# Optimization experiments

Hardware: AMD Instinct MI355X
Metric: run time of the kernel (lower is better)

## Reference

```python
import jax, jax.numpy as jnp
import numpy as np

D_MODEL = 1024
NUM_HEADS = 4
KEY_DIM = 1024      # dim * expand_k
VALUE_DIM = 2048    # dim * expand_v
HEAD_QK = KEY_DIM // NUM_HEADS   # 256
HEAD_V = VALUE_DIM // NUM_HEADS  # 512
EPS = 1e-5
ROPE_BASE = 10000.0
XAVIER_GAIN = 2.0 ** (-2.5)


def _xavier_uniform(key, shape, gain=XAVIER_GAIN):
    fan_in, fan_out = shape
    a = gain * np.sqrt(6.0 / (fan_in + fan_out))
    return jax.random.uniform(key, shape, jnp.float32, -a, a)


def setup_inputs() -> dict:
    key = jax.random.key(0)
    ks = jax.random.split(key, 5)
    x = jax.random.normal(ks[0], (2, 2048, D_MODEL), jnp.float32)
    # stored as (in, out); y = x @ W matches torch Linear(no bias) with W^T
    Wq = _xavier_uniform(ks[1], (D_MODEL, KEY_DIM))
    Wk = _xavier_uniform(ks[2], (D_MODEL, KEY_DIM))
    Wv = _xavier_uniform(ks[3], (D_MODEL, VALUE_DIM))
    Wo = _xavier_uniform(ks[4], (VALUE_DIM, D_MODEL))
    return {"x": x, "Wq": Wq, "Wk": Wk, "Wv": Wv, "Wo": Wo}


def _rope(t, base=ROPE_BASE):
    # t: [b, n, h, d]; standard half-split rotary embedding
    n, d = t.shape[1], t.shape[-1]
    half = d // 2
    inv_freq = 1.0 / (base ** (jnp.arange(0, half, dtype=jnp.float32) * 2.0 / d))
    ang = jnp.arange(n, dtype=jnp.float32)[:, None] * inv_freq  # [n, d/2]
    cos = jnp.cos(ang)[None, :, None, :]
    sin = jnp.sin(ang)[None, :, None, :]
    t1, t2 = t[..., :half], t[..., half:]
    return jnp.concatenate([t1 * cos - t2 * sin, t2 * cos + t1 * sin], axis=-1)


def reference(x, Wq, Wk, Wv, Wo):
    b, n, _ = x.shape
    # projections: b n (h d) -> b (n) h d
    q = (x @ Wq).reshape(b, n, NUM_HEADS, HEAD_QK)
    k = (x @ Wk).reshape(b, n, NUM_HEADS, HEAD_QK)
    v = (x @ Wv).reshape(b, n, NUM_HEADS, HEAD_V).transpose(0, 2, 1, 3)  # b h n dv
    q = _rope(q).transpose(0, 2, 1, 3)  # b h n dk
    k = _rope(k).transpose(0, 2, 1, 3)
    scale = HEAD_QK ** (-0.5)
    exp_qk = jnp.tril(jnp.exp(jnp.einsum('bhid,bhjd->bhij', q, k) * scale))
    exp_kk = jnp.tril(jnp.exp(jnp.einsum('bhid,bhjd->bhij', k, k) * scale))
    A = exp_kk.astype(jnp.float32) + EPS * jnp.eye(n, dtype=jnp.float32)
    sol = jax.lax.linalg.triangular_solve(A, v.astype(jnp.float32),
                                          left_side=True, lower=True)
    o = exp_qk.astype(jnp.float32) @ sol                # b h n dv
    o = o.transpose(0, 2, 1, 3).reshape(b, n, VALUE_DIM)  # b n (h dv)
    return o.astype(x.dtype) @ Wo
```

## Files before the change

### kernel.cpp

```cpp
#include <hip/hip_runtime.h>
#include <hip/hip_bf16.h>
#include <math.h>

#define SEQ   2048
#define NROW  4096
#define DM    1024
#define LDQ   1024
#define LDV   2048
#define NBLK  16

typedef float  f32x4  __attribute__((ext_vector_type(4)));
typedef int    i32x4  __attribute__((ext_vector_type(4)));
typedef __bf16 bf16x8 __attribute__((ext_vector_type(8)));

#define MFMA(d, a, b) (d) = __builtin_amdgcn_mfma_f32_16x16x32_bf16((a), (b), (d), 0, 0, 0)

__device__ inline ushort f2bf(float f) {
  __hip_bfloat16 h = __float2bfloat16(f);
  return *(ushort*)&h;
}
__device__ inline float bf2f(ushort u) {
  return __uint_as_float((unsigned)u << 16);
}
__device__ inline void split2(float v, ushort& hi, ushort& lo) {
  hi = f2bf(v);
  lo = f2bf(v - bf2f(hi));
}
__device__ inline bf16x8 ldfrag(const ushort* p) { return *(const bf16x8*)p; }

__global__ void pack_x_kernel(const float* __restrict__ X, ushort* __restrict__ P)
{
  const int t = blockIdx.x * 256 + threadIdx.x;
  const int kc = t & 127;
  const int m  = t >> 7;
  const float* src = X + (size_t)m * DM + kc * 8;
  f32x4 v0 = *(const f32x4*)src;
  f32x4 v1 = *(const f32x4*)(src + 4);
  ushort o[8];
  #pragma unroll
  for (int j = 0; j < 4; ++j) { o[j] = f2bf(v0[j]); o[4 + j] = f2bf(v1[j]); }
  ushort* dst = P + ((size_t)((m >> 7) * 128 + kc) * 128 + (m & 127)) * 8;
  *(i32x4*)dst = *(i32x4*)o;
}

__global__ void pack_w_kernel(const float* __restrict__ W, ushort* __restrict__ P,
                              int K, int N)
{
  const int K8 = K >> 3;
  const int t = blockIdx.x * 256 + threadIdx.x;
  const int c  = t & 127;
  const int kc = (t >> 7) % K8;
  const int nb = t / (128 * K8);
  ushort o[8];
  #pragma unroll
  for (int j = 0; j < 8; ++j)
    o[j] = f2bf(W[(size_t)(kc * 8 + j) * N + nb * 128 + c]);
  ushort* dst = P + ((size_t)(nb * K8 + kc) * 128 + c) * 8;
  *(i32x4*)dst = *(i32x4*)o;
}

__global__ void rope_pack1_kernel(const float* __restrict__ M,
                                  ushort* __restrict__ Phi, ushort* __restrict__ Plo)
{
  const int idx = blockIdx.x * 256 + threadIdx.x;
  const int g   = idx & 31;
  const int h   = (idx >> 5) & 3;
  const int row = idx >> 7;
  const int pos = row & (SEQ - 1);
  const int d0  = g * 8;
  const bool hihalf = d0 >= 128;
  const int f0 = d0 & 127;
  const float* mp = M + (size_t)row * LDQ + h * 256;
  ushort oh[8], ol[8];
  #pragma unroll
  for (int j = 0; j < 8; ++j) {
    const int f = f0 + j;
    const float inv = expf(-(float)f * (9.210340371976184f / 128.f));
    float s, c;
    sincosf((float)pos * inv, &s, &c);
    const float m1 = mp[f], m2 = mp[f + 128];
    const float mv = hihalf ? (m2 * c + m1 * s) : (m1 * c - m2 * s);
    split2(mv, oh[j], ol[j]);
  }
  const int b = row >> 11, r = row & 127, tb = (row & 2047) >> 7;
  const int bh = b * 4 + h;
  const size_t doff = (((size_t)(bh * 16 + tb) * 32 + g) * 128 + r) * 8;
  *(i32x4*)(Phi + doff) = *(i32x4*)oh;
  *(i32x4*)(Plo + doff) = *(i32x4*)ol;
}

__global__ void pack_sol_kernel(const float* __restrict__ Vb, ushort* __restrict__ Sp)
{
  const int hj = blockIdx.x;
  const int h  = hj >> 4, jb = hj & 15;
  const int c  = blockIdx.y * 256 + threadIdx.x;
  const float* src = Vb + (size_t)(jb * 128) * LDV + h * 512 + c;
  ushort* dhi = Sp + ((size_t)hj * 2    ) * 65536;
  ushort* dlo = Sp + ((size_t)hj * 2 + 1) * 65536;
  for (int kc = 0; kc < 16; ++kc) {
    ushort oh[8], ol[8];
    #pragma unroll
    for (int j = 0; j < 8; ++j)
      split2(src[(size_t)(kc * 8 + j) * LDV], oh[j], ol[j]);
    *(i32x4*)(dhi + ((size_t)kc * 512 + c) * 8) = *(i32x4*)oh;
    *(i32x4*)(dlo + ((size_t)kc * 512 + c) * 8) = *(i32x4*)ol;
  }
}

__global__ __launch_bounds__(256) void gemm_bf16(
    const ushort* __restrict__ Ap, const ushort* __restrict__ Bp,
    float* __restrict__ C, int M, int N, int K)
{
  __shared__ __align__(16) ushort a_lds[8][128][8];
  __shared__ __align__(16) ushort b_lds[8][128][8];
  const int tid  = threadIdx.x;
  const int lane = tid & 63;
  const int w    = tid >> 6;
  const int wr   = w >> 1, wc = w & 1;
  const int mb = blockIdx.y, nb = blockIdx.x;
  const int K8 = K >> 3;
  const ushort* aT = Ap + (size_t)mb * K8 * 1024;
  const ushort* bT = Bp + (size_t)nb * K8 * 1024;
  const int lr = lane & 15;
  const int lk = lane >> 4;

  f32x4 acc[4][4];
  #pragma unroll
  for (int i = 0; i < 4; ++i)
    #pragma unroll
    for (int j = 0; j < 4; ++j) acc[i][j] = (f32x4)(0.f);

  for (int kc0 = 0; kc0 < K8; kc0 += 8) {
    i32x4 av[4], bv[4];
    const ushort* asrc = aT + (size_t)kc0 * 1024;
    const ushort* bsrc = bT + (size_t)kc0 * 1024;
    #pragma unroll
    for (int it = 0; it < 4; ++it) {
      av[it] = *(const i32x4*)(asrc + it * 2048 + tid * 8);
      bv[it] = *(const i32x4*)(bsrc + it * 2048 + tid * 8);
    }
    __syncthreads();
    #pragma unroll
    for (int it = 0; it < 4; ++it) {
      *(i32x4*)((ushort*)a_lds + it * 2048 + tid * 8) = av[it];
      *(i32x4*)((ushort*)b_lds + it * 2048 + tid * 8) = bv[it];
    }
    __syncthreads();
    #pragma unroll
    for (int kk = 0; kk < 2; ++kk) {
      bf16x8 af[4], bf[4];
      #pragma unroll
      for (int m = 0; m < 4; ++m)
        af[m] = ldfrag(&a_lds[kk * 4 + lk][wr * 64 + m * 16 + lr][0]);
      #pragma unroll
      for (int n = 0; n < 4; ++n)
        bf[n] = ldfrag(&b_lds[kk * 4 + lk][wc * 64 + n * 16 + lr][0]);
      #pragma unroll
      for (int m = 0; m < 4; ++m)
        #pragma unroll
        for (int n = 0; n < 4; ++n)
          MFMA(acc[m][n], af[m], bf[n]);
    }
  }
  const int r0 = (lane >> 4) * 4;
  #pragma unroll
  for (int m = 0; m < 4; ++m)
    #pragma unroll
    for (int n = 0; n < 4; ++n) {
      const int row = mb * 128 + wr * 64 + m * 16 + r0;
      const int col = nb * 128 + wc * 64 + n * 16 + lr;
      float* cp = C + (size_t)row * N + col;
      #pragma unroll
      for (int q = 0; q < 4; ++q) cp[(size_t)q * N] = acc[m][n][q];
    }
}

__global__ __launch_bounds__(256) void winv_kernel(
    const ushort* __restrict__ Khi, const ushort* __restrict__ Klo,
    ushort* __restrict__ Whi, ushort* __restrict__ Wlo)
{
  __shared__ float L[128][129];
  __shared__ float W[128][129];
  const int t = blockIdx.x, bh = blockIdx.y;
  const int tid = threadIdx.x;
  const int lane = tid & 63, w = tid >> 6;
  const int wr = w >> 1, wc = w & 1;
  const int lr = lane & 15, lk = lane >> 4;
  const size_t kb = (size_t)(bh * 16 + t) * 32768;

  f32x4 acc[4][4];
  #pragma unroll
  for (int i = 0; i < 4; ++i)
    #pragma unroll
    for (int j = 0; j < 4; ++j) acc[i][j] = (f32x4)(0.f);
  #pragma unroll
  for (int ks = 0; ks < 8; ++ks) {
    bf16x8 ah[4], al[4];
    #pragma unroll
    for (int m = 0; m < 4; ++m) {
      const size_t off = kb + ((size_t)(ks * 4 + lk) * 128 + wr * 64 + m * 16 + lr) * 8;
      ah[m] = ldfrag(Khi + off);
      al[m] = ldfrag(Klo + off);
    }
    #pragma unroll
    for (int n = 0; n < 4; ++n) {
      const size_t off = kb + ((size_t)(ks * 4 + lk) * 128 + wc * 64 + n * 16 + lr) * 8;
      bf16x8 bh_ = ldfrag(Khi + off);
      bf16x8 bl_ = ldfrag(Klo + off);
      #pragma unroll
      for (int m = 0; m < 4; ++m) {
        MFMA(acc[m][n], ah[m], bh_);
        MFMA(acc[m][n], ah[m], bl_);
        MFMA(acc[m][n], al[m], bh_);
      }
    }
  }
  for (int i = tid; i < 128 * 129; i += 256) ((float*)W)[i] = 0.f;
  #pragma unroll
  for (int m = 0; m < 4; ++m)
    #pragma unroll
    for (int n = 0; n < 4; ++n)
      #pragma unroll
      for (int q = 0; q < 4; ++q) {
        const int row = wr * 64 + m * 16 + lk * 4 + q;
        const int col = wc * 64 + n * 16 + lr;
        float v = __expf(acc[m][n][q] * 0.0625f);
        if (row == col) v += 1e-5f;
        L[row][col] = v;
      }
  __syncthreads();
  if (tid < 128) {
    const int c = tid;
    W[c][c] = 1.f / L[c][c];
    for (int r = c + 1; r < 128; ++r) {
      float s0 = 0.f, s1 = 0.f, s2 = 0.f, s3 = 0.f;
      int j = c;
      for (; j + 4 <= r; j += 4) {
        s0 += L[r][j]     * W[j][c];
        s1 += L[r][j + 1] * W[j + 1][c];
        s2 += L[r][j + 2] * W[j + 2][c];
        s3 += L[r][j + 3] * W[j + 3][c];
      }
      for (; j < r; ++j) s0 += L[r][j] * W[j][c];
      W[r][c] = -((s0 + s1) + (s2 + s3)) / L[r][r];
    }
  }
  __syncthreads();
  const size_t wb = (size_t)(bh * 16 + t) * 16384;
  for (int i = tid; i < 2048; i += 256) {
    const int kc = i >> 7, r = i & 127;
    ushort oh[8], ol[8];
    #pragma unroll
    for (int j = 0; j < 8; ++j) split2(W[r][kc * 8 + j], oh[j], ol[j]);
    *(i32x4*)(Whi + wb + (size_t)i * 8) = *(i32x4*)oh;
    *(i32x4*)(Wlo + wb + (size_t)i * 8) = *(i32x4*)ol;
  }
}

__global__ __launch_bounds__(512) void apply_w0_kernel(
    const ushort* __restrict__ Whi, const ushort* __restrict__ Wlo,
    float* __restrict__ V, ushort* __restrict__ SR)
{
  __shared__ __align__(16) ushort shi[16 * 128 * 8];
  __shared__ __align__(16) ushort slo[16 * 128 * 8];
  const int cs = blockIdx.x, bh = blockIdx.y;
  const int b = bh >> 2, h = bh & 3;
  const int tid = threadIdx.x;
  const int lane = tid & 63, w = tid >> 6;
  const int wr = w >> 2, wc = w & 3, lr = lane & 15, lk = lane >> 4;
  const size_t wb = (size_t)(bh * 16) * 16384;
  float* Vrows = V + (size_t)b * SEQ * LDV + h * 512;
  ushort* srw = SR + (size_t)bh * 131072;

  for (int e = 0; e < 2; ++e) {
    const int cc = cs * 2 + e;
    if (e) __syncthreads();
    {
      const int k = tid >> 2, c0 = (tid & 3) * 32;
      const float* vp = Vrows + (size_t)k * LDV + cc * 128 + c0;
      for (int c = 0; c < 32; ++c) {
        ushort hi, lo;
        split2(vp[c], hi, lo);
        const int idx = (((k >> 3) * 128) + c0 + c) * 8 + (k & 7);
        shi[idx] = hi; slo[idx] = lo;
      }
    }
    __syncthreads();
    f32x4 acc[4][2];
    #pragma unroll
    for (int i = 0; i < 4; ++i)
      #pragma unroll
      for (int j = 0; j < 2; ++j) acc[i][j] = (f32x4)(0.f);
    #pragma unroll
    for (int ks = 0; ks < 4; ++ks) {
      bf16x8 ah[4], al[4];
      #pragma unroll
      for (int m = 0; m < 4; ++m) {
        const size_t off = wb + ((size_t)(ks * 4 + lk) * 128 + wr * 64 + m * 16 + lr) * 8;
        ah[m] = ldfrag(Whi + off);
        al[m] = ldfrag(Wlo + off);
      }
      #pragma unroll
      for (int n = 0; n < 2; ++n) {
        const int idx = (((ks * 4 + lk) * 128) + wc * 32 + n * 16 + lr) * 8;
        bf16x8 bh_ = ldfrag(&shi[idx]);
        bf16x8 bl_ = ldfrag(&slo[idx]);
        #pragma unroll
        for (int m = 0; m < 4; ++m) {
          MFMA(acc[m][n], ah[m], bh_);
          MFMA(acc[m][n], ah[m], bl_);
          MFMA(acc[m][n], al[m], bh_);
        }
      }
    }
    #pragma unroll
    for (int m = 0; m < 4; ++m)
      #pragma unroll
      for (int n = 0; n < 2; ++n) {
        const int col = wc * 32 + n * 16 + lr;
        #pragma unroll
        for (int q = 0; q < 4; ++q) {
          const int row = wr * 64 + m * 16 + lk * 4 + q;
          const float v = acc[m][n][q];
          Vrows[(size_t)row * LDV + cc * 128 + col] = v;
          ushort hi, lo;
          split2(v, hi, lo);
          const size_t so = ((size_t)(row >> 3) * 512 + cc * 128 + col) * 8 + (row & 7);
          srw[so] = hi; srw[65536 + so] = lo;
        }
      }
  }
}

__global__ __launch_bounds__(512) void solve_step_kernel(
    const ushort* __restrict__ Khi, const ushort* __restrict__ Klo,
    const ushort* __restrict__ Whi, const ushort* __restrict__ Wlo,
    float* __restrict__ V, ushort* __restrict__ SR, int t)
{
  __shared__ __align__(16) ushort pAhi[16 * 128 * 8];
  __shared__ __align__(16) ushort pAlo[16 * 128 * 8];
  __shared__ __align__(16) ushort rhshi[16 * 128 * 8];
  __shared__ __align__(16) ushort rhslo[16 * 128 * 8];
  const int ib = t + 1 + blockIdx.x;
  const int cs = blockIdx.y;
  const int bh = blockIdx.z;
  const int b = bh >> 2, h = bh & 3;
  const bool lead = (blockIdx.x == 0);
  const int tid = threadIdx.x;
  const int lane = tid & 63, w = tid >> 6;
  const int wr = w >> 2, wc = w & 3, lr = lane & 15, lk = lane >> 4;
  const size_t kbi = (size_t)(bh * 16 + ib) * 32768;
  const size_t kbt = (size_t)(bh * 16 + t) * 32768;
  float* Vhead = V + (size_t)b * SEQ * LDV + h * 512;
  float* Vib = Vhead + (size_t)ib * 128 * LDV;
  const ushort* srr = SR + (size_t)(t & 1) * 1048576 + (size_t)bh * 131072;
  ushort* srw       = SR + (size_t)((t + 1) & 1) * 1048576 + (size_t)bh * 131072;

  {
    f32x4 a1[4][2];
    #pragma unroll
    for (int i = 0; i < 4; ++i)
      #pragma unroll
      for (int j = 0; j < 2; ++j) a1[i][j] = (f32x4)(0.f);
    #pragma unroll
    for (int ks = 0; ks < 8; ++ks) {
      bf16x8 ah[4], al[4];
      #pragma unroll
      for (int m = 0; m < 4; ++m) {
        const size_t off = kbi + ((size_t)(ks * 4 + lk) * 128 + wr * 64 + m * 16 + lr) * 8;
        ah[m] = ldfrag(Khi + off);
        al[m] = ldfrag(Klo + off);
      }
      #pragma unroll
      for (int n = 0; n < 2; ++n) {
        const size_t off = kbt + ((size_t)(ks * 4 + lk) * 128 + wc * 32 + n * 16 + lr) * 8;
        bf16x8 bh_ = ldfrag(Khi + off);
        bf16x8 bl_ = ldfrag(Klo + off);
        #pragma unroll
        for (int m = 0; m < 4; ++m) {
          MFMA(a1[m][n], ah[m], bh_);
          MFMA(a1[m][n], ah[m], bl_);
          MFMA(a1[m][n], al[m], bh_);
        }
      }
    }
    #pragma unroll
    for (int m = 0; m < 4; ++m)
      #pragma unroll
      for (int n = 0; n < 2; ++n)
        #pragma unroll
        for (int q = 0; q < 4; ++q) {
          const int row = wr * 64 + m * 16 + lk * 4 + q;
          const int c   = wc * 32 + n * 16 + lr;
          const float e = __expf(a1[m][n][q] * 0.0625f);
          ushort hi, lo;
          split2(e, hi, lo);
          const int idx = (((c >> 3) * 128) + row) * 8 + (c & 7);
          pAhi[idx] = hi; pAlo[idx] = lo;
        }
  }
  __syncthreads();

  for (int e = 0; e < 2; ++e) {
    const int cc = cs * 2 + e;
    f32x4 u[4][2];
    #pragma unroll
    for (int i = 0; i < 4; ++i)
      #pragma unroll
      for (int j = 0; j < 2; ++j) u[i][j] = (f32x4)(0.f);
    #pragma unroll
    for (int ks = 0; ks < 4; ++ks) {
      bf16x8 ah[4], al[4];
      #pragma unroll
      for (int m = 0; m < 4; ++m) {
        const int idx = (((ks * 4 + lk) * 128) + wr * 64 + m * 16 + lr) * 8;
        ah[m] = ldfrag(&pAhi[idx]);
        al[m] = ldfrag(&pAlo[idx]);
      }
      #pragma unroll
      for (int n = 0; n < 2; ++n) {
        const size_t c = cc * 128 + wc * 32 + n * 16 + lr;
        bf16x8 bh_ = ldfrag(srr + ((size_t)(ks * 4 + lk) * 512 + c) * 8);
        bf16x8 bl_ = ldfrag(srr + 65536 + ((size_t)(ks * 4 + lk) * 512 + c) * 8);
        #pragma unroll
        for (int m = 0; m < 4; ++m) {
          MFMA(u[m][n], ah[m], bh_);
          MFMA(u[m][n], ah[m], bl_);
          MFMA(u[m][n], al[m], bh_);
        }
      }
    }
    float nv[4][2][4];
    #pragma unroll
    for (int m = 0; m < 4; ++m)
      #pragma unroll
      for (int n = 0; n < 2; ++n) {
        const int col = wc * 32 + n * 16 + lr;
        #pragma unroll
        for (int q = 0; q < 4; ++q) {
          const int row = wr * 64 + m * 16 + lk * 4 + q;
          const float v = Vib[(size_t)row * LDV + cc * 128 + col] - u[m][n][q];
          nv[m][n][q] = v;
          if (!lead) Vib[(size_t)row * LDV + cc * 128 + col] = v;
        }
      }
    if (lead) {
      __syncthreads();
      #pragma unroll
      for (int m = 0; m < 4; ++m)
        #pragma unroll
        for (int n = 0; n < 2; ++n) {
          const int col = wc * 32 + n * 16 + lr;
          #pragma unroll
          for (int q = 0; q < 4; ++q) {
            const int row = wr * 64 + m * 16 + lk * 4 + q;
            ushort hi, lo;
            split2(nv[m][n][q], hi, lo);
            const int idx = (((row >> 3) * 128) + col) * 8 + (row & 7);
            rhshi[idx] = hi; rhslo[idx] = lo;
          }
        }
      __syncthreads();
      f32x4 s2[4][2];
      #pragma unroll
      for (int i = 0; i < 4; ++i)
        #pragma unroll
        for (int j = 0; j < 2; ++j) s2[i][j] = (f32x4)(0.f);
      const size_t wb = (size_t)(bh * 16 + ib) * 16384;
      #pragma unroll
      for (int ks = 0; ks < 4; ++ks) {
        bf16x8 ah[4], al[4];
        #pragma unroll
        for (int m = 0; m < 4; ++m) {
          const size_t off = wb + ((size_t)(ks * 4 + lk) * 128 + wr * 64 + m * 16 + lr) * 8;
          ah[m] = ldfrag(Whi + off);
          al[m] = ldfrag(Wlo + off);
        }
        #pragma unroll
        for (int n = 0; n < 2; ++n) {
          const int idx = (((ks * 4 + lk) * 128) + wc * 32 + n * 16 + lr) * 8;
          bf16x8 bh_ = ldfrag(&rhshi[idx]);
          bf16x8 bl_ = ldfrag(&rhslo[idx]);
          #pragma unroll
          for (int m = 0; m < 4; ++m) {
            MFMA(s2[m][n], ah[m], bh_);
            MFMA(s2[m][n], ah[m], bl_);
            MFMA(s2[m][n], al[m], bh_);
          }
        }
      }
      #pragma unroll
      for (int m = 0; m < 4; ++m)
        #pragma unroll
        for (int n = 0; n < 2; ++n) {
          const int col = wc * 32 + n * 16 + lr;
          #pragma unroll
          for (int q = 0; q < 4; ++q) {
            const int row = wr * 64 + m * 16 + lk * 4 + q;
            const float v = s2[m][n][q];
            Vib[(size_t)row * LDV + cc * 128 + col] = v;
            ushort hi, lo;
            split2(v, hi, lo);
            const size_t so = ((size_t)(row >> 3) * 512 + cc * 128 + col) * 8 + (row & 7);
            srw[so] = hi; srw[65536 + so] = lo;
          }
        }
    }
  }
}

__global__ __launch_bounds__(512) void o_kernel(
    const ushort* __restrict__ Qhi, const ushort* __restrict__ Qlo,
    const ushort* __restrict__ Khi, const ushort* __restrict__ Klo,
    const ushort* __restrict__ Sp0, const ushort* __restrict__ Sp1,
    ushort* __restrict__ Opack)
{
  __shared__ __align__(16) ushort Phi_s[16 * 128 * 8];
  __shared__ __align__(16) ushort Plo_s[16 * 128 * 8];
  const int bid = blockIdx.x;
  const int bh  = bid & 7;
  const int cq  = (bid >> 3) & 3;
  const int ib  = 15 - (bid >> 5);
  const int b = bh >> 2, h = bh & 3;
  const int tid = threadIdx.x;
  const int lane = tid & 63, w = tid >> 6;
  const int wr = w >> 2, wc = w & 3, lr = lane & 15, lk = lane >> 4;
  const ushort* Spb = b ? Sp1 : Sp0;

  const size_t qb = (size_t)(bh * 16 + ib) * 32768;
  f32x4 acc[4][2];
  #pragma unroll
  for (int i = 0; i < 4; ++i)
    #pragma unroll
    for (int j = 0; j < 2; ++j) acc[i][j] = (f32x4)(0.f);

  for (int jb = 0; jb <= ib; ++jb) {
    f32x4 s1[4][2];
    #pragma unroll
    for (int i = 0; i < 4; ++i)
      #pragma unroll
      for (int j = 0; j < 2; ++j) s1[i][j] = (f32x4)(0.f);
    const size_t kb = (size_t)(bh * 16 + jb) * 32768;
    #pragma unroll
    for (int ks = 0; ks < 8; ++ks) {
      bf16x8 ah[4], al[4];
      #pragma unroll
      for (int m = 0; m < 4; ++m) {
        const size_t off = qb + ((size_t)(ks * 4 + lk) * 128 + wr * 64 + m * 16 + lr) * 8;
        ah[m] = ldfrag(Qhi + off);
        al[m] = ldfrag(Qlo + off);
      }
      #pragma unroll
      for (int n = 0; n < 2; ++n) {
        const size_t off = kb + ((size_t)(ks * 4 + lk) * 128 + wc * 32 + n * 16 + lr) * 8;
        bf16x8 bh_ = ldfrag(Khi + off);
        bf16x8 bl_ = ldfrag(Klo + off);
        #pragma unroll
        for (int m = 0; m < 4; ++m) {
          MFMA(s1[m][n], ah[m], bh_);
          MFMA(s1[m][n], ah[m], bl_);
          MFMA(s1[m][n], al[m], bh_);
        }
      }
    }
    if (jb) __syncthreads();
    #pragma unroll
    for (int m = 0; m < 4; ++m)
      #pragma unroll
      for (int n = 0; n < 2; ++n)
        #pragma unroll
        for (int q = 0; q < 4; ++q) {
          const int row = wr * 64 + m * 16 + lk * 4 + q;
          const int c   = wc * 32 + n * 16 + lr;
          float e = __expf(s1[m][n][q] * 0.0625f);
          if (jb == ib && c > row) e = 0.f;
          ushort hi, lo;
          split2(e, hi, lo);
          const int idx = (((c >> 3) * 128) + row) * 8 + (c & 7);
          Phi_s[idx] = hi; Plo_s[idx] = lo;
        }
    __syncthreads();
    const ushort* sjb = Spb + ((size_t)(h * 16 + jb) * 2) * 65536;
    #pragma unroll
    for (int ks = 0; ks < 4; ++ks) {
      bf16x8 ah[4], al[4];
      #pragma unroll
      for (int m = 0; m < 4; ++m) {
        const int idx = (((ks * 4 + lk) * 128) + wr * 64 + m * 16 + lr) * 8;
        ah[m] = ldfrag(&Phi_s[idx]);
        al[m] = ldfrag(&Plo_s[idx]);
      }
      #pragma unroll
      for (int n = 0; n < 2; ++n) {
        const size_t c = cq * 128 + wc * 32 + n * 16 + lr;
        bf16x8 bh_ = ldfrag(sjb + ((size_t)(ks * 4 + lk) * 512 + c) * 8);
        bf16x8 bl_ = ldfrag(sjb + 65536 + ((size_t)(ks * 4 + lk) * 512 + c) * 8);
        #pragma unroll
        for (int m = 0; m < 4; ++m) {
          MFMA(acc[m][n], ah[m], bh_);
          MFMA(acc[m][n], ah[m], bl_);
          MFMA(acc[m][n], al[m], bh_);
        }
      }
    }
  }
  const int row_blk = b * 16 + ib;
  #pragma unroll
  for (int m = 0; m < 4; ++m)
    #pragma unroll
    for (int n = 0; n < 2; ++n) {
      const int col = h * 512 + cq * 128 + wc * 32 + n * 16 + lr;
      #pragma unroll
      for (int q = 0; q < 4; ++q) {
        const int row = wr * 64 + m * 16 + lk * 4 + q;
        Opack[((size_t)row_blk * 256 + (col >> 3)) * 1024 + row * 8 + (col & 7)] =
            f2bf(acc[m][n][q]);
      }
    }
}

extern "C" void kernel_launch(void* const* d_in, const int* in_sizes, int n_in,
                              void* d_out, int out_size, void* d_ws, size_t ws_size,
                              hipStream_t stream)
{
  const float* x  = (const float*)d_in[0];
  const float* Wq = (const float*)d_in[1];
  const float* Wk = (const float*)d_in[2];
  const float* Wv = (const float*)d_in[3];
  const float* Wo = (const float*)d_in[4];
  float* out = (float*)d_out;

  char* base = (char*)d_ws;
  ushort* xpack = (ushort*)(base);
  ushort* Wqp   = (ushort*)(base + (8u  << 20));
  ushort* Wkp   = (ushort*)(base + (10u << 20));
  ushort* Wvp   = (ushort*)(base + (12u << 20));
  ushort* Wop   = (ushort*)(base + (16u << 20));
  float*  Q     = (float*) (base + (20u << 20));
  float*  K     = (float*) (base + (36u << 20));
  float*  V     = (float*) (base + (52u << 20));
  ushort* Qhi   = (ushort*)(base);
  ushort* Qlo   = (ushort*)(base + (8u  << 20));
  ushort* Khi   = (ushort*)(base + (20u << 20));
  ushort* Klo   = (ushort*)(base + (28u << 20));
  ushort* Whi   = (ushort*)(base + (36u << 20));
  ushort* Wlo   = (ushort*)(base + (40u << 20));
  ushort* SR    = (ushort*)(base + (44u << 20));
  ushort* Sp1   = (ushort*)(base + (36u << 20));
  ushort* Sp0   = (ushort*)(base + (68u << 20));
  ushort* Opack = (ushort*)(base + (52u << 20));

  pack_x_kernel<<<(NROW * 128) / 256, 256, 0, stream>>>(x, xpack);
  pack_w_kernel<<<(1024 * 1024 / 8) / 256, 256, 0, stream>>>(Wq, Wqp, 1024, 1024);
  pack_w_kernel<<<(1024 * 1024 / 8) / 256, 256, 0, stream>>>(Wk, Wkp, 1024, 1024);
  pack_w_kernel<<<(1024 * 2048 / 8) / 256, 256, 0, stream>>>(Wv, Wvp, 1024, 2048);
  pack_w_kernel<<<(2048 * 1024 / 8) / 256, 256, 0, stream>>>(Wo, Wop, 2048, 1024);

  gemm_bf16<<<dim3(DM / 128, NROW / 128), 256, 0, stream>>>(xpack, Wqp, Q, NROW, DM, DM);
  gemm_bf16<<<dim3(DM / 128, NROW / 128), 256, 0, stream>>>(xpack, Wkp, K, NROW, DM, DM);
  gemm_bf16<<<dim3(LDV / 128, NROW / 128), 256, 0, stream>>>(xpack, Wvp, V, NROW, LDV, DM);

  rope_pack1_kernel<<<(NROW * 4 * 32) / 256, 256, 0, stream>>>(Q, Qhi, Qlo);
  rope_pack1_kernel<<<(NROW * 4 * 32) / 256, 256, 0, stream>>>(K, Khi, Klo);

  winv_kernel<<<dim3(NBLK, 8), 256, 0, stream>>>(Khi, Klo, Whi, Wlo);
  apply_w0_kernel<<<dim3(2, 8), 512, 0, stream>>>(Whi, Wlo, V, SR);
  for (int t = 0; t < NBLK - 1; ++t)
    solve_step_kernel<<<dim3(NBLK - 1 - t, 2, 8), 512, 0, stream>>>(Khi, Klo, Whi, Wlo, V, SR, t);

  pack_sol_kernel<<<dim3(64, 2), 256, 0, stream>>>(V + (size_t)SEQ * LDV, Sp1);
  pack_sol_kernel<<<dim3(64, 2), 256, 0, stream>>>(V, Sp0);

  o_kernel<<<512, 512, 0, stream>>>(Qhi, Qlo, Khi, Klo, Sp0, Sp1, Opack);

  gemm_bf16<<<dim3(DM / 128, NROW / 128), 256, 0, stream>>>(Opack, Wop, out, NROW, DM, LDV);
}
```

Baseline: 1.478 ms.

## Split solve column chunks across more blocks and use direct global-to-LDS loads in GEMM

The apply_w0 and solve_step kernels now launch one block per 128-column chunk instead of looping over two chunks per block, doubling grid parallelism on the latency-bound sequential solve. The solve_step kernel also reuses the pA LDS buffers for the RHS, cutting shared memory per block, which may help occupancy. Separately, the GEMM stages tiles with global_load_lds instead of going through registers. The trade-off is recomputing the pA panel in every block, so the pA setup work is done twice as often overall.

```diff
diff --git a/kernel.cpp b/kernel.cpp
--- a/kernel.cpp
+++ b/kernel.cpp
@@ -27,6 +27,12 @@
   lo = f2bf(v - bf2f(hi));
 }
 __device__ inline bf16x8 ldfrag(const ushort* p) { return *(const bf16x8*)p; }
+
+__device__ inline void gload_lds16(const ushort* g, ushort* l) {
+  __builtin_amdgcn_global_load_lds(
+      (const __attribute__((address_space(1))) void*)g,
+      (__attribute__((address_space(3))) void*)l, 16, 0, 0);
+}
 
 __global__ void pack_x_kernel(const float* __restrict__ X, ushort* __restrict__ P)
 {
@@ -131,19 +137,13 @@
     for (int j = 0; j < 4; ++j) acc[i][j] = (f32x4)(0.f);
 
   for (int kc0 = 0; kc0 < K8; kc0 += 8) {
-    i32x4 av[4], bv[4];
     const ushort* asrc = aT + (size_t)kc0 * 1024;
     const ushort* bsrc = bT + (size_t)kc0 * 1024;
+    __syncthreads();
     #pragma unroll
     for (int it = 0; it < 4; ++it) {
-      av[it] = *(const i32x4*)(asrc + it * 2048 + tid * 8);
-      bv[it] = *(const i32x4*)(bsrc + it * 2048 + tid * 8);
-    }
-    __syncthreads();
-    #pragma unroll
-    for (int it = 0; it < 4; ++it) {
-      *(i32x4*)((ushort*)a_lds + it * 2048 + tid * 8) = av[it];
-      *(i32x4*)((ushort*)b_lds + it * 2048 + tid * 8) = bv[it];
+      gload_lds16(asrc + it * 2048 + tid * 8, ((ushort*)a_lds) + it * 2048 + tid * 8);
+      gload_lds16(bsrc + it * 2048 + tid * 8, ((ushort*)b_lds) + it * 2048 + tid * 8);
     }
     __syncthreads();
     #pragma unroll
@@ -263,7 +263,7 @@
 {
   __shared__ __align__(16) ushort shi[16 * 128 * 8];
   __shared__ __align__(16) ushort slo[16 * 128 * 8];
-  const int cs = blockIdx.x, bh = blockIdx.y;
+  const int cc = blockIdx.x, bh = blockIdx.y;
   const int b = bh >> 2, h = bh & 3;
   const int tid = threadIdx.x;
   const int lane = tid & 63, w = tid >> 6;
@@ -272,64 +272,60 @@
   float* Vrows = V + (size_t)b * SEQ * LDV + h * 512;
   ushort* srw = SR + (size_t)bh * 131072;
 
-  for (int e = 0; e < 2; ++e) {
-    const int cc = cs * 2 + e;
-    if (e) __syncthreads();
-    {
-      const int k = tid >> 2, c0 = (tid & 3) * 32;
-      const float* vp = Vrows + (size_t)k * LDV + cc * 128 + c0;
-      for (int c = 0; c < 32; ++c) {
+  {
+    const int k = tid >> 2, c0 = (tid & 3) * 32;
+    const float* vp = Vrows + (size_t)k * LDV + cc * 128 + c0;
+    for (int c = 0; c < 32; ++c) {
+      ushort hi, lo;
+      split2(vp[c], hi, lo);
+      const int idx = (((k >> 3) * 128) + c0 + c) * 8 + (k & 7);
+      shi[idx] = hi; slo[idx] = lo;
+    }
+  }
+  __syncthreads();
+  f32x4 acc[4][2];
+  #pragma unroll
+  for (int i = 0; i < 4; ++i)
+    #pragma unroll
+    for (int j = 0; j < 2; ++j) acc[i][j] = (f32x4)(0.f);
+  #pragma unroll
+  for (int ks = 0; ks < 4; ++ks) {
+    bf16x8 ah[4], al[4];
+    #pragma unroll
+    for (int m = 0; m < 4; ++m) {
+      const size_t off = wb + ((size_t)(ks * 4 + lk) * 128 + wr * 64 + m * 16 + lr) * 8;
+      ah[m] = ldfrag(Whi + off);
+      al[m] = ldfrag(Wlo + off);
+    }
+    #pragma unroll
+    for (int n = 0; n < 2; ++n) {
+      const int idx = (((ks * 4 + lk) * 128) + wc * 32 + n * 16 + lr) * 8;
+      bf16x8 bh_ = ldfrag(&shi[idx]);
+      bf16x8 bl_ = ldfrag(&slo[idx]);
+      #pragma unroll
+      for (int m = 0; m < 4; ++m) {
+        MFMA(acc[m][n], ah[m], bh_);
+        MFMA(acc[m][n], ah[m], bl_);
+        MFMA(acc[m][n], al[m], bh_);
+      }
+    }
+  }
+  #pragma unroll
+  for (int m = 0; m < 4; ++m)
+    #pragma unroll
+    for (int n = 0; n < 2; ++n) {
+      const int col = wc * 32 + n * 16 + lr;
+      #pragma unroll
+      for (int q = 0; q < 4; ++q) {
+        const int row = wr * 64 + m * 16 + lk * 4 + q;
+        const float v = acc[m][n][q];
+        Vrows[(size_t)row * LDV + cc * 128 + col] = v;
         ushort hi, lo;
-        split2(vp[c], hi, lo);
-        const int idx = (((k >> 3) * 128) + c0 + c) * 8 + (k & 7);
-        shi[idx] = hi; slo[idx] = lo;
-      }
-    }
-    __syncthreads();
-    f32x4 acc[4][2];
-    #pragma unroll
-    for (int i = 0; i < 4; ++i)
-      #pragma unroll
-      for (int j = 0; j < 2; ++j) acc[i][j] = (f32x4)(0.f);
-    #pragma unroll
-    for (int ks = 0; ks < 4; ++ks) {
-      bf16x8 ah[4], al[4];
-      #pragma unroll
-      for (int m = 0; m < 4; ++m) {
-        const size_t off = wb + ((size_t)(ks * 4 + lk) * 128 + wr * 64 + m * 16 + lr) * 8;
-        ah[m] = ldfrag(Whi + off);
-        al[m] = ldfrag(Wlo + off);
-      }
-      #pragma unroll
-      for (int n = 0; n < 2; ++n) {
-        const int idx = (((ks * 4 + lk) * 128) + wc * 32 + n * 16 + lr) * 8;
-        bf16x8 bh_ = ldfrag(&shi[idx]);
-        bf16x8 bl_ = ldfrag(&slo[idx]);
-        #pragma unroll
-        for (int m = 0; m < 4; ++m) {
-          MFMA(acc[m][n], ah[m], bh_);
-          MFMA(acc[m][n], ah[m], bl_);
-          MFMA(acc[m][n], al[m], bh_);
-        }
-      }
-    }
-    #pragma unroll
-    for (int m = 0; m < 4; ++m)
-      #pragma unroll
-      for (int n = 0; n < 2; ++n) {
-        const int col = wc * 32 + n * 16 + lr;
-        #pragma unroll
-        for (int q = 0; q < 4; ++q) {
-          const int row = wr * 64 + m * 16 + lk * 4 + q;
-          const float v = acc[m][n][q];
-          Vrows[(size_t)row * LDV + cc * 128 + col] = v;
-          ushort hi, lo;
-          split2(v, hi, lo);
-          const size_t so = ((size_t)(row >> 3) * 512 + cc * 128 + col) * 8 + (row & 7);
-          srw[so] = hi; srw[65536 + so] = lo;
-        }
-      }
-  }
+        split2(v, hi, lo);
+        const size_t so = ((size_t)(row >> 3) * 512 + cc * 128 + col) * 8 + (row & 7);
+        srw[so] = hi; srw[65536 + so] = lo;
+      }
+    }
 }
 
 __global__ __launch_bounds__(512) void solve_step_kernel(
@@ -339,10 +335,8 @@
 {
   __shared__ __align__(16) ushort pAhi[16 * 128 * 8];
   __shared__ __align__(16) ushort pAlo[16 * 128 * 8];
-  __shared__ __align__(16) ushort rhshi[16 * 128 * 8];
-  __shared__ __align__(16) ushort rhslo[16 * 128 * 8];
   const int ib = t + 1 + blockIdx.x;
-  const int cs = blockIdx.y;
+  const int cc = blockIdx.y;
   const int bh = blockIdx.z;
   const int b = bh >> 2, h = bh & 3;
   const bool lead = (blockIdx.x == 0);
@@ -401,36 +395,92 @@
   }
   __syncthreads();
 
-  for (int e = 0; e < 2; ++e) {
-    const int cc = cs * 2 + e;
-    f32x4 u[4][2];
+  f32x4 u[4][2];
+  #pragma unroll
+  for (int i = 0; i < 4; ++i)
+    #pragma unroll
+    for (int j = 0; j < 2; ++j) u[i][j] = (f32x4)(0.f);
+  #pragma unroll
+  for (int ks = 0; ks < 4; ++ks) {
+    bf16x8 ah[4], al[4];
+    #pragma unroll
+    for (int m = 0; m < 4; ++m) {
+      const int idx = (((ks * 4 + lk) * 128) + wr * 64 + m * 16 + lr) * 8;
+      ah[m] = ldfrag(&pAhi[idx]);
+      al[m] = ldfrag(&pAlo[idx]);
+    }
+    #pragma unroll
+    for (int n = 0; n < 2; ++n) {
+      const size_t c = cc * 128 + wc * 32 + n * 16 + lr;
+      bf16x8 bh_ = ldfrag(srr + ((size_t)(ks * 4 + lk) * 512 + c) * 8);
+      bf16x8 bl_ = ldfrag(srr + 65536 + ((size_t)(ks * 4 + lk) * 512 + c) * 8);
+      #pragma unroll
+      for (int m = 0; m < 4; ++m) {
+        MFMA(u[m][n], ah[m], bh_);
+        MFMA(u[m][n], ah[m], bl_);
+        MFMA(u[m][n], al[m], bh_);
+      }
+    }
+  }
+  float nv[4][2][4];
+  #pragma unroll
+  for (int m = 0; m < 4; ++m)
+    #pragma unroll
+    for (int n = 0; n < 2; ++n) {
+      const int col = wc * 32 + n * 16 + lr;
+      #pragma unroll
+      for (int q = 0; q < 4; ++q) {
+        const int row = wr * 64 + m * 16 + lk * 4 + q;
+        const float v = Vib[(size_t)row * LDV + cc * 128 + col] - u[m][n][q];
+        nv[m][n][q] = v;
+        if (!lead) Vib[(size_t)row * LDV + cc * 128 + col] = v;
+      }
+    }
+  if (lead) {
+    __syncthreads();
+    #pragma unroll
+    for (int m = 0; m < 4; ++m)
+      #pragma unroll
+      for (int n = 0; n < 2; ++n) {
+        const int col = wc * 32 + n * 16 + lr;
+        #pragma unroll
+        for (int q = 0; q < 4; ++q) {
+          const int row = wr * 64 + m * 16 + lk * 4 + q;
+          ushort hi, lo;
+          split2(nv[m][n][q], hi, lo);
+          const int idx = (((row >> 3) * 128) + col) * 8 + (row & 7);
+          pAhi[idx] = hi; pAlo[idx] = lo;
+        }
+      }
+    __syncthreads();
+    f32x4 s2[4][2];
     #pragma unroll
     for (int i = 0; i < 4; ++i)
       #pragma unroll
-      for (int j = 0; j < 2; ++j) u[i][j] = (f32x4)(0.f);
+      for (int j = 0; j < 2; ++j) s2[i][j] = (f32x4)(0.f);
+    const size_t wb = (size_t)(bh * 16 + ib) * 16384;
     #pragma unroll
     for (int ks = 0; ks < 4; ++ks) {
       bf16x8 ah[4], al[4];
       #pragma unroll
       for (int m = 0; m < 4; ++m) {
-        const int idx = (((ks * 4 + lk) * 128) + wr * 64 + m * 16 + lr) * 8;
-        ah[m] = ldfrag(&pAhi[idx]);
-        al[m] = ldfrag(&pAlo[idx]);
+        const size_t off = wb + ((size_t)(ks * 4 + lk) * 128 + wr * 64 + m * 16 + lr) * 8;
+        ah[m] = ldfrag(Whi + off);
+        al[m] = ldfrag(Wlo + off);
       }
       #pragma unroll
       for (int n = 0; n < 2; ++n) {
-        const size_t c = cc * 128 + wc * 32 + n * 16 + lr;
-        bf16x8 bh_ = ldfrag(srr + ((size_t)(ks * 4 + lk) * 512 + c) * 8);
-        bf16x8 bl_ = ldfrag(srr + 65536 + ((size_t)(ks * 4 + lk) * 512 + c) * 8);
+        const int idx = (((ks * 4 + lk) * 128) + wc * 32 + n * 16 + lr) * 8;
+        bf16x8 bh_ = ldfrag(&pAhi[idx]);
+        bf16x8 bl_ = ldfrag(&pAlo[idx]);
         #pragma unroll
         for (int m = 0; m < 4; ++m) {
-          MFMA(u[m][n], ah[m], bh_);
-          MFMA(u[m][n], ah[m], bl_);
-          MFMA(u[m][n], al[m], bh_);
-        }
-      }
-    }
-    float nv[4][2][4];
+          MFMA(s2[m][n], ah[m], bh_);
+          MFMA(s2[m][n], ah[m], bl_);
+          MFMA(s2[m][n], al[m], bh_);
+        }
+      }
+    }
     #pragma unroll
     for (int m = 0; m < 4; ++m)
       #pragma unroll
@@ -439,73 +489,14 @@
         #pragma unroll
         for (int q = 0; q < 4; ++q) {
           const int row = wr * 64 + m * 16 + lk * 4 + q;
-          const float v = Vib[(size_t)row * LDV + cc * 128 + col] - u[m][n][q];
-          nv[m][n][q] = v;
-          if (!lead) Vib[(size_t)row * LDV + cc * 128 + col] = v;
-        }
-      }
-    if (lead) {
-      __syncthreads();
-      #pragma unroll
-      for (int m = 0; m < 4; ++m)
-        #pragma unroll
-        for (int n = 0; n < 2; ++n) {
-          const int col = wc * 32 + n * 16 + lr;
-          #pragma unroll
-          for (int q = 0; q < 4; ++q) {
-            const int row = wr * 64 + m * 16 + lk * 4 + q;
-            ushort hi, lo;
-            split2(nv[m][n][q], hi, lo);
-            const int idx = (((row >> 3) * 128) + col) * 8 + (row & 7);
-            rhshi[idx] = hi; rhslo[idx] = lo;
-          }
-        }
-      __syncthreads();
-      f32x4 s2[4][2];
-      #pragma unroll
-      for (int i = 0; i < 4; ++i)
-        #pragma unroll
-        for (int j = 0; j < 2; ++j) s2[i][j] = (f32x4)(0.f);
-      const size_t wb = (size_t)(bh * 16 + ib) * 16384;
-      #pragma unroll
-      for (int ks = 0; ks < 4; ++ks) {
-        bf16x8 ah[4], al[4];
-        #pragma unroll
-        for (int m = 0; m < 4; ++m) {
-          const size_t off = wb + ((size_t)(ks * 4 + lk) * 128 + wr * 64 + m * 16 + lr) * 8;
-          ah[m] = ldfrag(Whi + off);
-          al[m] = ldfrag(Wlo + off);
-        }
-        #pragma unroll
-        for (int n = 0; n < 2; ++n) {
-          const int idx = (((ks * 4 + lk) * 128) + wc * 32 + n * 16 + lr) * 8;
-          bf16x8 bh_ = ldfrag(&rhshi[idx]);
-          bf16x8 bl_ = ldfrag(&rhslo[idx]);
-          #pragma unroll
-          for (int m = 0; m < 4; ++m) {
-            MFMA(s2[m][n], ah[m], bh_);
-            MFMA(s2[m][n], ah[m], bl_);
-            MFMA(s2[m][n], al[m], bh_);
-          }
-        }
-      }
-      #pragma unroll
-      for (int m = 0; m < 4; ++m)
-        #pragma unroll
-        for (int n = 0; n < 2; ++n) {
-          const int col = wc * 32 + n * 16 + lr;
-          #pragma unroll
-          for (int q = 0; q < 4; ++q) {
-            const int row = wr * 64 + m * 16 + lk * 4 + q;
-            const float v = s2[m][n][q];
-            Vib[(size_t)row * LDV + cc * 128 + col] = v;
-            ushort hi, lo;
-            split2(v, hi, lo);
-            const size_t so = ((size_t)(row >> 3) * 512 + cc * 128 + col) * 8 + (row & 7);
-            srw[so] = hi; srw[65536 + so] = lo;
-          }
-        }
-    }
+          const float v = s2[m][n][q];
+          Vib[(size_t)row * LDV + cc * 128 + col] = v;
+          ushort hi, lo;
+          split2(v, hi, lo);
+          const size_t so = ((size_t)(row >> 3) * 512 + cc * 128 + col) * 8 + (row & 7);
+          srw[so] = hi; srw[65536 + so] = lo;
+        }
+      }
   }
 }
 
@@ -664,9 +655,9 @@
   rope_pack1_kernel<<<(NROW * 4 * 32) / 256, 256, 0, stream>>>(K, Khi, Klo);
 
   winv_kernel<<<dim3(NBLK, 8), 256, 0, stream>>>(Khi, Klo, Whi, Wlo);
-  apply_w0_kernel<<<dim3(2, 8), 512, 0, stream>>>(Whi, Wlo, V, SR);
+  apply_w0_kernel<<<dim3(4, 8), 512, 0, stream>>>(Whi, Wlo, V, SR);
   for (int t = 0; t < NBLK - 1; ++t)
-    solve_step_kernel<<<dim3(NBLK - 1 - t, 2, 8), 512, 0, stream>>>(Khi, Klo, Whi, Wlo, V, SR, t);
+    solve_step_kernel<<<dim3(NBLK - 1 - t, 4, 8), 512, 0, stream>>>(Khi, Klo, Whi, Wlo, V, SR, t);
 
   pack_sol_kernel<<<dim3(64, 2), 256, 0, stream>>>(V + (size_t)SEQ * LDV, Sp1);
   pack_sol_kernel<<<dim3(64, 2), 256, 0, stream>>>(V, Sp0);
```

New measurement: 1.314 ms. -11.1%, faster.
